# Performance work log

Hardware: AMD Instinct MI355X
Metric: run time of the kernel (lower is better)

## Reference

```python
import jax, jax.numpy as jnp
import numpy as np

B, T, E, D = 8, 2048, 1024, 64  # batch, seq_len, n_emb, head_dim

def setup_inputs() -> dict:
    key = jax.random.key(0)
    ks = jax.random.split(key, 4)
    scale = 1.0 / np.sqrt(E)
    return {
        "x": jax.random.normal(ks[0], (B, T, E), dtype=jnp.float32),
        "Wq": jax.random.normal(ks[1], (E, D), dtype=jnp.float32) * scale,
        "bq": jnp.zeros((D,), dtype=jnp.float32),
        "Wk": jax.random.normal(ks[2], (E, D), dtype=jnp.float32) * scale,
        "bk": jnp.zeros((D,), dtype=jnp.float32),
        "Wv": jax.random.normal(ks[3], (E, D), dtype=jnp.float32) * scale,
        "bv": jnp.zeros((D,), dtype=jnp.float32),
    }

def reference(x, Wq, bq, Wk, bk, Wv, bv):
    # QKV projections: [B,T,E] @ [E,D] -> [B,T,D]
    q = x @ Wq + bq
    k = x @ Wk + bk
    v = x @ Wv + bv
    d = q.shape[-1]
    # scaled dot-product scores [B,T,T]
    wei = jnp.einsum('btd,bsd->bts', q, k) * (d ** -0.5)
    # causal mask: position t attends to s <= t
    t = wei.shape[1]
    causal = jnp.tril(jnp.ones((t, t), dtype=bool))
    wei = jnp.where(causal, wei, -jnp.inf)
    wei = jax.nn.softmax(wei, axis=-1)
    # attention output [B,T,D]
    return jnp.einsum('bts,bsd->btd', wei, v)
```

## Files before the change

kernel.cpp:

```cpp
#include <hip/hip_runtime.h>
#include <math.h>


#define B_   8
#define T_   2048
#define E_   1024
#define D_   64
#define BT_  (B_ * T_)

typedef __attribute__((ext_vector_type(8))) short s16x8;
typedef __attribute__((ext_vector_type(4))) short s16x4;
typedef __attribute__((ext_vector_type(4))) float f32x4;

__device__ __forceinline__ short f2bf(float f) {
    union { float f; unsigned u; } a; a.f = f;
    unsigned r = a.u + 0x7fffu + ((a.u >> 16) & 1u);
    return (short)(r >> 16);
}

#define MFMA16(a, b, c) __builtin_amdgcn_mfma_f32_16x16x32_bf16((a), (b), (c), 0, 0, 0)

typedef __attribute__((address_space(1))) const unsigned int gu32;
typedef __attribute__((address_space(3)))       unsigned int su32;
__device__ __forceinline__ void gld16(const void* g, void* s) {
    __builtin_amdgcn_global_load_lds((gu32*)g, (su32*)s, 16, 0, 0);
}

#define DPPF(x, ctrl) __builtin_bit_cast(float, \
    __builtin_amdgcn_update_dpp(0, __builtin_bit_cast(int, (x)), (ctrl), 0xF, 0xF, true))

__device__ __forceinline__ float rsum16(float x) {
    x += DPPF(x, 0xB1);
    x += DPPF(x, 0x4E);
    x += DPPF(x, 0x124);
    x += DPPF(x, 0x128);
    return x;
}

__global__ __launch_bounds__(256) void wtrans_kernel(
    const float* __restrict__ Wq, const float* __restrict__ Wk,
    const float* __restrict__ Wv, short* __restrict__ Wt)
{
    __shared__ float sT[64][65];
    const int sel = blockIdx.x >> 4;
    const int k0  = (blockIdx.x & 15) * 64;
    const float* W = sel == 0 ? Wq : (sel == 1 ? Wk : Wv);
    const int t  = threadIdx.x;
    const int kr = t >> 4, c4 = (t & 15) * 4;
    #pragma unroll
    for (int i = 0; i < 4; ++i) {
        float4 v = *(const float4*)&W[(size_t)(k0 + kr + i * 16) * D_ + c4];
        sT[kr + i * 16][c4 + 0] = v.x; sT[kr + i * 16][c4 + 1] = v.y;
        sT[kr + i * 16][c4 + 2] = v.z; sT[kr + i * 16][c4 + 3] = v.w;
    }
    __syncthreads();
    #pragma unroll
    for (int i = 0; i < 4; ++i) {
        int n  = (t >> 4) + i * 16;
        int kk = (t & 15) * 4;
        s16x4 o;
        o.x = f2bf(sT[kk + 0][n]); o.y = f2bf(sT[kk + 1][n]);
        o.z = f2bf(sT[kk + 2][n]); o.w = f2bf(sT[kk + 3][n]);
        *(s16x4*)&Wt[(size_t)(sel * 64 + n) * E_ + k0 + kk] = o;
    }
}

__global__ __launch_bounds__(512) void qkv_kernel(
    const float* __restrict__ x, const short* __restrict__ Wt,
    const float* __restrict__ bq, const float* __restrict__ bk,
    const float* __restrict__ bv,
    short* __restrict__ Qg, short* __restrict__ Kg, short* __restrict__ VTg)
{
    __shared__ short sW[2][12 * 16 * 128];
    __shared__ short sX[2][64 * 140];
    const int tid  = threadIdx.x;
    const int lane = tid & 63;
    const int w    = tid >> 6;
    const int l15  = lane & 15, quad = lane >> 4;
    const int h2   = w & 1;
    const int n2   = w >> 1;
    const int t0   = blockIdx.x * 64;
    const int bb   = t0 >> 11;

    const int srow = tid >> 3;
    const int skc  = (tid & 7) * 16;
    const float* px = &x[(size_t)(t0 + srow) * E_ + skc];

    const int lrow = lane >> 4;
    const int lc16 = lane & 15;

    f32x4 acc[3][2];
    #pragma unroll
    for (int a = 0; a < 3; ++a)
        #pragma unroll
        for (int h = 0; h < 2; ++h)
            acc[a][h] = (f32x4){0.f, 0.f, 0.f, 0.f};

    float4 lda0 = *(const float4*)(px +   0);
    float4 lda1 = *(const float4*)(px +   4);
    float4 lda2 = *(const float4*)(px +   8);
    float4 lda3 = *(const float4*)(px +  12);
    float4 ldb0 = *(const float4*)(px + 128);
    float4 ldb1 = *(const float4*)(px + 132);
    float4 ldb2 = *(const float4*)(px + 136);
    float4 ldb3 = *(const float4*)(px + 140);

    #pragma unroll
    for (int j = 0; j < 6; ++j) {
        const int cid = w * 6 + j;
        const int t3g = cid >> 2;
        const int rr  = ((cid & 3) << 2) + lrow;
        const int c16 = lc16 ^ (rr & 7);
        gld16(&Wt[(size_t)(t3g * 16 + rr) * E_ + c16 * 8],
              (char*)&sW[0][0] + cid * 1024);
    }

    int buf = 0;
    for (int k0 = 0; k0 < E_; k0 += 128) {
        s16x8 pk0, pk1;
        pk0[0] = f2bf(lda0.x); pk0[1] = f2bf(lda0.y);
        pk0[2] = f2bf(lda0.z); pk0[3] = f2bf(lda0.w);
        pk0[4] = f2bf(lda1.x); pk0[5] = f2bf(lda1.y);
        pk0[6] = f2bf(lda1.z); pk0[7] = f2bf(lda1.w);
        pk1[0] = f2bf(lda2.x); pk1[1] = f2bf(lda2.y);
        pk1[2] = f2bf(lda2.z); pk1[3] = f2bf(lda2.w);
        pk1[4] = f2bf(lda3.x); pk1[5] = f2bf(lda3.y);
        pk1[6] = f2bf(lda3.z); pk1[7] = f2bf(lda3.w);
        *(s16x8*)&sX[buf][srow * 140 + skc]     = pk0;
        *(s16x8*)&sX[buf][srow * 140 + skc + 8] = pk1;
        __syncthreads();

        lda0 = ldb0; lda1 = ldb1; lda2 = ldb2; lda3 = ldb3;
        if (k0 + 256 < E_) {
            const float* p2 = px + k0 + 256;
            ldb0 = *(const float4*)(p2 +  0);
            ldb1 = *(const float4*)(p2 +  4);
            ldb2 = *(const float4*)(p2 +  8);
            ldb3 = *(const float4*)(p2 + 12);
        }
        if (k0 + 128 < E_) {
            #pragma unroll
            for (int j = 0; j < 6; ++j) {
                const int cid = w * 6 + j;
                const int t3g = cid >> 2;
                const int rr  = ((cid & 3) << 2) + lrow;
                const int c16 = lc16 ^ (rr & 7);
                gld16(&Wt[(size_t)(t3g * 16 + rr) * E_ + k0 + 128 + c16 * 8],
                      (char*)&sW[buf ^ 1][0] + cid * 1024);
            }
        }

        s16x8 aw[3][4];
        #pragma unroll
        for (int t3 = 0; t3 < 3; ++t3) {
            const int tb = (n2 * 3 + t3) * 2048 + l15 * 128;
            #pragma unroll
            for (int kc = 0; kc < 4; ++kc) {
                const int c16 = (kc * 4 + quad) ^ (l15 & 7);
                aw[t3][kc] = *(const s16x8*)&sW[buf][tb + c16 * 8];
            }
        }
        s16x8 bxf[2][4];
        #pragma unroll
        for (int h = 0; h < 2; ++h) {
            const int trow = (h2 * 2 + h) * 16 + l15;
            #pragma unroll
            for (int kc = 0; kc < 4; ++kc)
                bxf[h][kc] = *(const s16x8*)&sX[buf][trow * 140 + kc * 32 + quad * 8];
        }
        #pragma unroll
        for (int t3 = 0; t3 < 3; ++t3)
            #pragma unroll
            for (int h = 0; h < 2; ++h)
                #pragma unroll
                for (int kc = 0; kc < 4; ++kc)
                    acc[t3][h] = MFMA16(aw[t3][kc], bxf[h][kc], acc[t3][h]);
        buf ^= 1;
    }

    __syncthreads();
    short* sVT = &sX[0][0];

    #pragma unroll
    for (int t3 = 0; t3 < 3; ++t3) {
        const int nt = n2 * 3 + t3;
        const int fb = (nt & 3) * 16 + quad * 4;
        const float* bias = nt < 4 ? bq : (nt < 8 ? bk : bv);
        f32x4 bsv = *(const f32x4*)&bias[fb];
        #pragma unroll
        for (int h = 0; h < 2; ++h) {
            const int lt  = (h2 * 2 + h) * 16 + l15;
            const int tok = t0 + lt;
            f32x4 v = acc[t3][h] + bsv;
            if (nt < 4) {
                v *= 0.125f;
                s16x4 o = { f2bf(v[0]), f2bf(v[1]), f2bf(v[2]), f2bf(v[3]) };
                *(s16x4*)&Qg[(size_t)tok * D_ + fb] = o;
            } else if (nt < 8) {
                s16x4 o = { f2bf(v[0]), f2bf(v[1]), f2bf(v[2]), f2bf(v[3]) };
                *(s16x4*)&Kg[(size_t)tok * D_ + fb] = o;
            } else {
                #pragma unroll
                for (int r = 0; r < 4; ++r)
                    sVT[(fb + r) * 72 + lt] = f2bf(v[r]);
            }
        }
    }
    __syncthreads();
    {
        const int d  = tid >> 3;
        const int tq = (tid & 7) * 8;
        s16x8 vv = *(const s16x8*)&sVT[d * 72 + tq];
        *(s16x8*)&VTg[(size_t)(bb * D_ + d) * T_ + (t0 & (T_ - 1)) + tq] = vv;
    }
}

__global__ __launch_bounds__(512) void attn_kernel(
    const short* __restrict__ Qg, const short* __restrict__ Kg,
    const short* __restrict__ VTg, float* __restrict__ out)
{
    __shared__ char smem[74752];
    short* sP = (short*)smem;
    float* sO = (float*)smem;
    float* sl = (float*)(smem + 73728);

    const int tid  = threadIdx.x;
    const int lane = tid & 63;
    const int w    = tid >> 6;
    const int l15  = lane & 15, quad = lane >> 4;
    const int b    = blockIdx.x & 7;
    const int j    = blockIdx.x >> 3;
    const int tq   = j * 32;
    const int nch  = (j >> 1) + 1;
    const int c0   = (w * nch) >> 3;
    const int c1   = ((w + 1) * nch) >> 3;

    s16x8 aq[2][2];
    #pragma unroll
    for (int qt = 0; qt < 2; ++qt) {
        const size_t qoff = ((size_t)b * T_ + tq + qt * 16 + l15) * D_ + quad * 8;
        aq[qt][0] = *(const s16x8*)&Qg[qoff];
        aq[qt][1] = *(const s16x8*)&Qg[qoff + 32];
    }

    f32x4 oo[2][4];
    float lp[2][4];
    #pragma unroll
    for (int qt = 0; qt < 2; ++qt) {
        #pragma unroll
        for (int nt = 0; nt < 4; ++nt)
            oo[qt][nt] = (f32x4){0.f, 0.f, 0.f, 0.f};
        #pragma unroll
        for (int r = 0; r < 4; ++r) lp[qt][r] = 0.f;
    }

    const short* kb = Kg  + (size_t)b * T_ * D_;
    const short* vb = VTg + (size_t)b * D_ * T_;
    short* sPw = sP + w * (2 * 16 * 72);

    for (int cc = c0; cc < c1; ++cc) {
        const int s0 = cc * 64;
        s16x8 bk[4][2];
        #pragma unroll
        for (int nt = 0; nt < 4; ++nt) {
            const short* pk = kb + (size_t)(s0 + nt * 16 + l15) * D_ + quad * 8;
            bk[nt][0] = *(const s16x8*)pk;
            bk[nt][1] = *(const s16x8*)(pk + 32);
        }
        const f32x4 zz = (f32x4){0.f, 0.f, 0.f, 0.f};
        f32x4 sacc[2][4];
        #pragma unroll
        for (int qt = 0; qt < 2; ++qt)
            #pragma unroll
            for (int nt = 0; nt < 4; ++nt) {
                sacc[qt][nt] = MFMA16(aq[qt][0], bk[nt][0], zz);
                sacc[qt][nt] = MFMA16(aq[qt][1], bk[nt][1], sacc[qt][nt]);
            }
        s16x8 bv[4][2];
        #pragma unroll
        for (int nt = 0; nt < 4; ++nt) {
            const short* pv = vb + (size_t)(nt * 16 + l15) * T_ + s0 + quad * 8;
            bv[nt][0] = *(const s16x8*)pv;
            bv[nt][1] = *(const s16x8*)(pv + 32);
        }
        const bool diag = (cc == nch - 1);
        float p[2][4][4];
        #pragma unroll
        for (int qt = 0; qt < 2; ++qt)
            #pragma unroll
            for (int nt = 0; nt < 4; ++nt)
                #pragma unroll
                for (int r = 0; r < 4; ++r) {
                    float e = __expf(sacc[qt][nt][r]);
                    if (diag && (s0 + nt * 16 + l15 > tq + qt * 16 + quad * 4 + r))
                        e = 0.f;
                    p[qt][nt][r] = e;
                }
        #pragma unroll
        for (int qt = 0; qt < 2; ++qt)
            #pragma unroll
            for (int r = 0; r < 4; ++r)
                lp[qt][r] += (p[qt][0][r] + p[qt][1][r]) + (p[qt][2][r] + p[qt][3][r]);
        #pragma unroll
        for (int qt = 0; qt < 2; ++qt)
            #pragma unroll
            for (int nt = 0; nt < 4; ++nt)
                #pragma unroll
                for (int r = 0; r < 4; ++r)
                    sPw[qt * (16 * 72) + (quad * 4 + r) * 72 + nt * 16 + l15] =
                        f2bf(p[qt][nt][r]);
        #pragma unroll
        for (int qt = 0; qt < 2; ++qt) {
            s16x8 ap0 = *(const s16x8*)&sPw[qt * (16 * 72) + l15 * 72 + quad * 8];
            s16x8 ap1 = *(const s16x8*)&sPw[qt * (16 * 72) + l15 * 72 + 32 + quad * 8];
            #pragma unroll
            for (int nt = 0; nt < 4; ++nt) {
                oo[qt][nt] = MFMA16(ap0, bv[nt][0], oo[qt][nt]);
                oo[qt][nt] = MFMA16(ap1, bv[nt][1], oo[qt][nt]);
            }
        }
    }

    f32x4 lv[2];
    #pragma unroll
    for (int qt = 0; qt < 2; ++qt)
        #pragma unroll
        for (int r = 0; r < 4; ++r)
            lv[qt][r] = rsum16(lp[qt][r]);

    __syncthreads();
    {
        float* sOw = sO + w * (64 * 36);
        #pragma unroll
        for (int qt = 0; qt < 2; ++qt)
            #pragma unroll
            for (int nt = 0; nt < 4; ++nt)
                *(f32x4*)&sOw[(nt * 16 + l15) * 36 + qt * 16 + quad * 4] = oo[qt][nt];
        if (l15 == 0) {
            *(f32x4*)&sl[w * 32 + quad * 4]      = lv[0];
            *(f32x4*)&sl[w * 32 + 16 + quad * 4] = lv[1];
        }
    }
    __syncthreads();
    {
        const int d  = tid & 63;
        const int rb = (tid >> 6) * 4;
        f32x4 osum = (f32x4){0.f, 0.f, 0.f, 0.f};
        f32x4 lsum = (f32x4){0.f, 0.f, 0.f, 0.f};
        #pragma unroll
        for (int w2 = 0; w2 < 8; ++w2) {
            osum += *(const f32x4*)&sO[w2 * (64 * 36) + d * 36 + rb];
            lsum += *(const f32x4*)&sl[w2 * 32 + rb];
        }
        #pragma unroll
        for (int i = 0; i < 4; ++i)
            out[((size_t)b * T_ + tq + rb + i) * D_ + d] = osum[i] / lsum[i];
    }
}

extern "C" void kernel_launch(void* const* d_in, const int* in_sizes, int n_in,
                              void* d_out, int out_size, void* d_ws, size_t ws_size,
                              hipStream_t stream) {
    (void)in_sizes; (void)n_in; (void)out_size; (void)ws_size;
    const float* x  = (const float*)d_in[0];
    const float* Wq = (const float*)d_in[1];
    const float* bq = (const float*)d_in[2];
    const float* Wk = (const float*)d_in[3];
    const float* bk = (const float*)d_in[4];
    const float* Wv = (const float*)d_in[5];
    const float* bv = (const float*)d_in[6];

    char* ws = (char*)d_ws;
    short* Qg  = (short*)(ws);
    short* Kg  = (short*)(ws + (size_t)2 * 1024 * 1024);
    short* VTg = (short*)(ws + (size_t)4 * 1024 * 1024);
    short* Wt  = (short*)(ws + (size_t)6 * 1024 * 1024);

    wtrans_kernel<<<48, 256, 0, stream>>>(Wq, Wk, Wv, Wt);
    qkv_kernel<<<BT_ / 64, 512, 0, stream>>>(x, Wt, bq, bk, bv, Qg, Kg, VTg);
    attn_kernel<<<B_ * 64, 512, 0, stream>>>(Qg, Kg, VTg, (float*)d_out);
}
```

Before: 141.1 us.

## Double attention query tile to 64 rows per block, halving grid size

Each attention block now handles 64 query rows instead of 32, so every K/V chunk loaded per wave is reused across four 16-row query tiles instead of two. The score, exp and P-store work is interleaved per query tile to limit live registers. The grid drops from 512 to 256 blocks and LDS grows to about 138 KB per block, which risks lower occupancy and fewer blocks than compute units on a 256-CU part, plus more causal-load imbalance.

Result: faster. 135.3 us (-4.1%).

```diff
diff --git a/kernel.cpp b/kernel.cpp
--- a/kernel.cpp
+++ b/kernel.cpp
@@ -219,10 +219,10 @@
     const short* __restrict__ Qg, const short* __restrict__ Kg,
     const short* __restrict__ VTg, float* __restrict__ out)
 {
-    __shared__ char smem[74752];
+    __shared__ char smem[141312];
     short* sP = (short*)smem;
     float* sO = (float*)smem;
-    float* sl = (float*)(smem + 73728);
+    float* sl = (float*)(smem + 139264);
 
     const int tid  = threadIdx.x;
     const int lane = tid & 63;
@@ -230,23 +230,23 @@
     const int l15  = lane & 15, quad = lane >> 4;
     const int b    = blockIdx.x & 7;
     const int j    = blockIdx.x >> 3;
-    const int tq   = j * 32;
-    const int nch  = (j >> 1) + 1;
+    const int tq   = j * 64;
+    const int nch  = j + 1;
     const int c0   = (w * nch) >> 3;
     const int c1   = ((w + 1) * nch) >> 3;
 
-    s16x8 aq[2][2];
-    #pragma unroll
-    for (int qt = 0; qt < 2; ++qt) {
+    s16x8 aq[4][2];
+    #pragma unroll
+    for (int qt = 0; qt < 4; ++qt) {
         const size_t qoff = ((size_t)b * T_ + tq + qt * 16 + l15) * D_ + quad * 8;
         aq[qt][0] = *(const s16x8*)&Qg[qoff];
         aq[qt][1] = *(const s16x8*)&Qg[qoff + 32];
     }
 
-    f32x4 oo[2][4];
-    float lp[2][4];
-    #pragma unroll
-    for (int qt = 0; qt < 2; ++qt) {
+    f32x4 oo[4][4];
+    float lp[4][4];
+    #pragma unroll
+    for (int qt = 0; qt < 4; ++qt) {
         #pragma unroll
         for (int nt = 0; nt < 4; ++nt)
             oo[qt][nt] = (f32x4){0.f, 0.f, 0.f, 0.f};
@@ -256,10 +256,11 @@
 
     const short* kb = Kg  + (size_t)b * T_ * D_;
     const short* vb = VTg + (size_t)b * D_ * T_;
-    short* sPw = sP + w * (2 * 16 * 72);
+    short* sPw = sP + w * (4 * 16 * 72);
 
     for (int cc = c0; cc < c1; ++cc) {
         const int s0 = cc * 64;
+        const bool diag = (cc == nch - 1);
         s16x8 bk[4][2];
         #pragma unroll
         for (int nt = 0; nt < 4; ++nt) {
@@ -268,14 +269,34 @@
             bk[nt][1] = *(const s16x8*)(pk + 32);
         }
         const f32x4 zz = (f32x4){0.f, 0.f, 0.f, 0.f};
-        f32x4 sacc[2][4];
-        #pragma unroll
-        for (int qt = 0; qt < 2; ++qt)
+        #pragma unroll
+        for (int qt = 0; qt < 4; ++qt) {
+            f32x4 sacc[4];
             #pragma unroll
             for (int nt = 0; nt < 4; ++nt) {
-                sacc[qt][nt] = MFMA16(aq[qt][0], bk[nt][0], zz);
-                sacc[qt][nt] = MFMA16(aq[qt][1], bk[nt][1], sacc[qt][nt]);
-            }
+                sacc[nt] = MFMA16(aq[qt][0], bk[nt][0], zz);
+                sacc[nt] = MFMA16(aq[qt][1], bk[nt][1], sacc[nt]);
+            }
+            float p[4][4];
+            #pragma unroll
+            for (int nt = 0; nt < 4; ++nt)
+                #pragma unroll
+                for (int r = 0; r < 4; ++r) {
+                    float e = __expf(sacc[nt][r]);
+                    if (diag && (s0 + nt * 16 + l15 > tq + qt * 16 + quad * 4 + r))
+                        e = 0.f;
+                    p[nt][r] = e;
+                }
+            #pragma unroll
+            for (int r = 0; r < 4; ++r)
+                lp[qt][r] += (p[0][r] + p[1][r]) + (p[2][r] + p[3][r]);
+            #pragma unroll
+            for (int nt = 0; nt < 4; ++nt)
+                #pragma unroll
+                for (int r = 0; r < 4; ++r)
+                    sPw[qt * (16 * 72) + (quad * 4 + r) * 72 + nt * 16 + l15] =
+                        f2bf(p[nt][r]);
+        }
         s16x8 bv[4][2];
         #pragma unroll
         for (int nt = 0; nt < 4; ++nt) {
@@ -283,34 +304,8 @@
             bv[nt][0] = *(const s16x8*)pv;
             bv[nt][1] = *(const s16x8*)(pv + 32);
         }
-        const bool diag = (cc == nch - 1);
-        float p[2][4][4];
-        #pragma unroll
-        for (int qt = 0; qt < 2; ++qt)
-            #pragma unroll
-            for (int nt = 0; nt < 4; ++nt)
-                #pragma unroll
-                for (int r = 0; r < 4; ++r) {
-                    float e = __expf(sacc[qt][nt][r]);
-                    if (diag && (s0 + nt * 16 + l15 > tq + qt * 16 + quad * 4 + r))
-                        e = 0.f;
-                    p[qt][nt][r] = e;
-                }
-        #pragma unroll
-        for (int qt = 0; qt < 2; ++qt)
-            #pragma unroll
-            for (int r = 0; r < 4; ++r)
-                lp[qt][r] += (p[qt][0][r] + p[qt][1][r]) + (p[qt][2][r] + p[qt][3][r]);
-        #pragma unroll
-        for (int qt = 0; qt < 2; ++qt)
-            #pragma unroll
-            for (int nt = 0; nt < 4; ++nt)
-                #pragma unroll
-                for (int r = 0; r < 4; ++r)
-                    sPw[qt * (16 * 72) + (quad * 4 + r) * 72 + nt * 16 + l15] =
-                        f2bf(p[qt][nt][r]);
-        #pragma unroll
-        for (int qt = 0; qt < 2; ++qt) {
+        #pragma unroll
+        for (int qt = 0; qt < 4; ++qt) {
             s16x8 ap0 = *(const s16x8*)&sPw[qt * (16 * 72) + l15 * 72 + quad * 8];
             s16x8 ap1 = *(const s16x8*)&sPw[qt * (16 * 72) + l15 * 72 + 32 + quad * 8];
             #pragma unroll
@@ -321,40 +316,50 @@
         }
     }
 
-    f32x4 lv[2];
-    #pragma unroll
-    for (int qt = 0; qt < 2; ++qt)
+    f32x4 lv[4];
+    #pragma unroll
+    for (int qt = 0; qt < 4; ++qt)
         #pragma unroll
         for (int r = 0; r < 4; ++r)
             lv[qt][r] = rsum16(lp[qt][r]);
 
     __syncthreads();
     {
-        float* sOw = sO + w * (64 * 36);
-        #pragma unroll
-        for (int qt = 0; qt < 2; ++qt)
+        float* sOw = sO + w * (64 * 68);
+        #pragma unroll
+        for (int qt = 0; qt < 4; ++qt)
             #pragma unroll
             for (int nt = 0; nt < 4; ++nt)
-                *(f32x4*)&sOw[(nt * 16 + l15) * 36 + qt * 16 + quad * 4] = oo[qt][nt];
+                *(f32x4*)&sOw[(nt * 16 + l15) * 68 + qt * 16 + quad * 4] = oo[qt][nt];
         if (l15 == 0) {
-            *(f32x4*)&sl[w * 32 + quad * 4]      = lv[0];
-            *(f32x4*)&sl[w * 32 + 16 + quad * 4] = lv[1];
+            #pragma unroll
+            for (int qt = 0; qt < 4; ++qt)
+                *(f32x4*)&sl[w * 64 + qt * 16 + quad * 4] = lv[qt];
         }
     }
     __syncthreads();
     {
         const int d  = tid & 63;
-        const int rb = (tid >> 6) * 4;
-        f32x4 osum = (f32x4){0.f, 0.f, 0.f, 0.f};
-        f32x4 lsum = (f32x4){0.f, 0.f, 0.f, 0.f};
+        const int rb = (tid >> 6) * 8;
+        f32x4 osum0 = (f32x4){0.f, 0.f, 0.f, 0.f};
+        f32x4 osum1 = (f32x4){0.f, 0.f, 0.f, 0.f};
+        f32x4 lsum0 = (f32x4){0.f, 0.f, 0.f, 0.f};
+        f32x4 lsum1 = (f32x4){0.f, 0.f, 0.f, 0.f};
         #pragma unroll
         for (int w2 = 0; w2 < 8; ++w2) {
-            osum += *(const f32x4*)&sO[w2 * (64 * 36) + d * 36 + rb];
-            lsum += *(const f32x4*)&sl[w2 * 32 + rb];
+            const float* so  = &sO[w2 * (64 * 68) + d * 68 + rb];
+            const float* slp = &sl[w2 * 64 + rb];
+            osum0 += *(const f32x4*)(so);
+            osum1 += *(const f32x4*)(so + 4);
+            lsum0 += *(const f32x4*)(slp);
+            lsum1 += *(const f32x4*)(slp + 4);
         }
         #pragma unroll
         for (int i = 0; i < 4; ++i)
-            out[((size_t)b * T_ + tq + rb + i) * D_ + d] = osum[i] / lsum[i];
+            out[((size_t)b * T_ + tq + rb + i) * D_ + d] = osum0[i] / lsum0[i];
+        #pragma unroll
+        for (int i = 0; i < 4; ++i)
+            out[((size_t)b * T_ + tq + rb + 4 + i) * D_ + d] = osum1[i] / lsum1[i];
     }
 }
 
@@ -378,5 +383,5 @@
 
     wtrans_kernel<<<48, 256, 0, stream>>>(Wq, Wk, Wv, Wt);
     qkv_kernel<<<BT_ / 64, 512, 0, stream>>>(x, Wt, bq, bk, bv, Qg, Kg, VTg);
-    attn_kernel<<<B_ * 64, 512, 0, stream>>>(Qg, Kg, VTg, (float*)d_out);
-}
+    attn_kernel<<<B_ * 32, 512, 0, stream>>>(Qg, Kg, VTg, (float*)d_out);
+}
```
